# Optimization experiments

Hardware: AMD Instinct MI355X
Metric: run time of the kernel (lower is better)

Reference implementation:

```python
import jax, jax.numpy as jnp
import numpy as np

# Module hyperparameters (init_kwargs)
TOP_K = 0.15          # fraction of pixels kept per row when step_percent=1
IGNORE_INDEX = 255

B, K, N, H, W = 8, 3, 8, 384, 384


def setup_inputs() -> dict:
    key = jax.random.key(0)
    k1, k2 = jax.random.split(key)
    # log-probabilities over K classes (nll_loss expects log-probs)
    logits = jax.random.normal(k1, (B, K, N, H, W), dtype=jnp.float32)
    inp = jax.nn.log_softmax(logits, axis=1)
    target = jax.random.randint(k2, (B, N, H, W), 0, K, dtype=jnp.int32)
    return {"input": inp, "target": target, "step_percent": 1}


def reference(input, target, step_percent):
    b, k, n, h, w = input.shape
    P = h * w
    x = input.reshape(b * n, k, P)           # (BN, K, P)
    t = target.reshape(b * n, P)             # (BN, P)

    # per-pixel NLL with ignore_index (ignored pixels contribute 0)
    mask = t != IGNORE_INDEX
    t_safe = jnp.where(mask, t, 0)
    nll = -jnp.take_along_axis(x, t_safe[:, None, :], axis=1)[:, 0, :]  # (BN, P)
    nll = jnp.where(mask, nll, jnp.zeros((), nll.dtype))

    # static k: step_percent is a Python scalar in the original forward
    sp = min(float(step_percent), 1.0)
    n_top_k = int(sp * TOP_K * P + (1.0 - sp) * P)

    top_k_loss, _ = jax.lax.top_k(nll, n_top_k)  # (BN, n_top_k)
    return jnp.mean(top_k_loss)
```

## Files before the change

### kernel.cpp

```cpp
#include <hip/hip_runtime.h>

#define BN   64
#define KCLS 3
#define PPIX 147456
#define NB1  4096
#define NB3  128
#define BLKS_PER_ROW 36
#define PX_PER_BLK   4096
#define F4_PER_BLK   1024
#define CAP  32768

static const size_t OFF_CAND = 0;
static const size_t OFF_C1   = OFF_CAND + (size_t)BN * CAP * 4;
static const size_t OFF_S1   = OFF_C1 + (size_t)BN * NB1 * 4;
static const size_t OFF_CCNT = OFF_S1 + (size_t)BN * NB1 * 4;
static const size_t OFF_B1   = OFF_CCNT + 256;
static const size_t OFF_R1   = OFF_B1 + 256;
static const size_t OFF_SS   = OFF_R1 + 256;
static const size_t OFF_ACC  = OFF_SS + 512;
static const size_t WS_END   = OFF_ACC + 8;

__device__ __forceinline__ unsigned topk_count(const int* sp_ptr) {
    double sp = (double)sp_ptr[0];
    if (sp > 1.0) sp = 1.0;
    return (unsigned)(sp * 0.15 * (double)PPIX + (1.0 - sp) * (double)PPIX);
}

__device__ __forceinline__ float sel_nll(int t, float a, float b, float c) {
    float lp = (t == 0) ? a : (t == 1) ? b : (t == 2) ? c : 0.0f;
    return fmaxf(-lp, 0.0f);
}

__global__ __launch_bounds__(256) void k_hist1(
    const float* __restrict__ in, const int* __restrict__ tgt,
    unsigned* __restrict__ cnt1, float* __restrict__ sum1)
{
    __shared__ unsigned lc[NB1];
    __shared__ float    ls[NB1];
    const int tid = threadIdx.x;
    for (int i = tid; i < NB1; i += 256) { lc[i] = 0u; ls[i] = 0.0f; }
    __syncthreads();

    const int row   = blockIdx.x / BLKS_PER_ROW;
    const int chunk = blockIdx.x % BLKS_PER_ROW;
    const float4* p0 = (const float4*)(in + (size_t)row * KCLS * PPIX);
    const float4* p1 = p0 + PPIX / 4;
    const float4* p2 = p1 + PPIX / 4;
    const int4*   t4 = (const int4*)(tgt + (size_t)row * PPIX);
    const int base = chunk * (F4_PER_BLK);

    #pragma unroll
    for (int j = 0; j < 4; ++j) {
        const int idx = base + j * 256 + tid;
        const int4   t = t4[idx];
        const float4 a = p0[idx];
        const float4 b = p1[idx];
        const float4 c = p2[idx];
        float v[4];
        v[0] = sel_nll(t.x, a.x, b.x, c.x);
        v[1] = sel_nll(t.y, a.y, b.y, c.y);
        v[2] = sel_nll(t.z, a.z, b.z, c.z);
        v[3] = sel_nll(t.w, a.w, b.w, c.w);
        #pragma unroll
        for (int q = 0; q < 4; ++q) {
            const unsigned key = __float_as_uint(v[q]) >> 19;
            atomicAdd(&lc[key], 1u);
            atomicAdd(&ls[key], v[q]);
        }
    }
    __syncthreads();

    unsigned* gc = cnt1 + (size_t)row * NB1;
    float*    gs = sum1 + (size_t)row * NB1;
    for (int i = tid; i < NB1; i += 256) {
        const unsigned cc = lc[i];
        if (cc) { atomicAdd(&gc[i], cc); atomicAdd(&gs[i], ls[i]); }
    }
}

__global__ __launch_bounds__(256) void k_scan(
    const unsigned* __restrict__ cnt, const float* __restrict__ sum,
    const int* __restrict__ sp_ptr, int* __restrict__ st_b, int* __restrict__ st_r,
    double* __restrict__ st_S)
{
    const int row = blockIdx.x, tid = threadIdx.x;
    __shared__ unsigned csum[256];
    __shared__ double   ssum[256];
    const unsigned* c = cnt + (size_t)row * NB1;
    const float*    s = sum + (size_t)row * NB1;

    unsigned cl[16]; float slv[16];
    unsigned cacc = 0; double sacc = 0.0;
    const int base = tid * 16;
    #pragma unroll
    for (int i = 0; i < 16; ++i) {
        const int bin = NB1 - 1 - (base + i);
        cl[i]  = c[bin];
        slv[i] = s[bin];
        cacc += cl[i];
        sacc += (double)slv[i];
    }
    csum[tid] = cacc; ssum[tid] = sacc;
    __syncthreads();
    for (int off = 1; off < 256; off <<= 1) {
        unsigned cv = 0; double sv = 0.0;
        if (tid >= off) { cv = csum[tid - off]; sv = ssum[tid - off]; }
        __syncthreads();
        csum[tid] += cv; ssum[tid] += sv;
        __syncthreads();
    }

    const unsigned k = topk_count(sp_ptr);
    unsigned cum = tid ? csum[tid - 1] : 0u;
    double   sS  = tid ? ssum[tid - 1] : 0.0;
    #pragma unroll
    for (int i = 0; i < 16; ++i) {
        const unsigned cb = cl[i];
        if (cum < k && cum + cb >= k) {
            st_b[row] = NB1 - 1 - (base + i);
            st_r[row] = (int)(k - cum);
            st_S[row] = sS;
        }
        cum += cb;
        sS  += (double)slv[i];
    }
}

__global__ __launch_bounds__(256) void k_compact(
    const float* __restrict__ in, const int* __restrict__ tgt,
    const int* __restrict__ st_b1, float* __restrict__ cand, int* __restrict__ ccnt)
{
    __shared__ float stage[PX_PER_BLK];
    __shared__ int lcnt, gbase;
    const int tid = threadIdx.x;
    if (tid == 0) lcnt = 0;
    __syncthreads();

    const int row   = blockIdx.x / BLKS_PER_ROW;
    const int chunk = blockIdx.x % BLKS_PER_ROW;
    const unsigned b1 = (unsigned)st_b1[row];
    const float4* p0 = (const float4*)(in + (size_t)row * KCLS * PPIX);
    const float4* p1 = p0 + PPIX / 4;
    const float4* p2 = p1 + PPIX / 4;
    const int4*   t4 = (const int4*)(tgt + (size_t)row * PPIX);
    const int base = chunk * (F4_PER_BLK);

    #pragma unroll
    for (int j = 0; j < 4; ++j) {
        const int idx = base + j * 256 + tid;
        const int4   t = t4[idx];
        const float4 a = p0[idx];
        const float4 b = p1[idx];
        const float4 c = p2[idx];
        float v[4];
        v[0] = sel_nll(t.x, a.x, b.x, c.x);
        v[1] = sel_nll(t.y, a.y, b.y, c.y);
        v[2] = sel_nll(t.z, a.z, b.z, c.z);
        v[3] = sel_nll(t.w, a.w, b.w, c.w);
        #pragma unroll
        for (int q = 0; q < 4; ++q) {
            if ((__float_as_uint(v[q]) >> 19) == b1) {
                const int s = atomicAdd(&lcnt, 1);
                stage[s] = v[q];
            }
        }
    }
    __syncthreads();
    if (tid == 0) gbase = atomicAdd(&ccnt[row], lcnt);
    __syncthreads();
    const int n = lcnt, gb = gbase;
    float* cr = cand + (size_t)row * CAP;
    for (int i = tid; i < n; i += 256) {
        const int pos = gb + i;
        if (pos < CAP) cr[pos] = stage[i];
    }
}

__global__ __launch_bounds__(256) void k_resolve(
    const float* __restrict__ cand, const int* __restrict__ ccnt,
    const int* __restrict__ st_b1, const int* __restrict__ st_r1,
    const double* __restrict__ st_S, double* __restrict__ accum)
{
    __shared__ unsigned lc[NB1];
    __shared__ float    ls[NB1];
    __shared__ unsigned csum[256];
    __shared__ double   ssum[256];
    __shared__ int sb2, sr2;
    __shared__ double sS2;

    const int row = blockIdx.x, tid = threadIdx.x;
    int n = ccnt[row]; if (n > CAP) n = CAP;
    const float* cv = cand + (size_t)row * CAP;

    for (int i = tid; i < NB1; i += 256) { lc[i] = 0u; ls[i] = 0.0f; }
    __syncthreads();
    for (int i = tid; i < n; i += 256) {
        const float v = cv[i];
        const unsigned key = (__float_as_uint(v) >> 7) & 0xFFFu;
        atomicAdd(&lc[key], 1u);
        atomicAdd(&ls[key], v);
    }
    __syncthreads();

    unsigned cl[16]; float slv[16];
    unsigned cacc = 0; double sacc = 0.0;
    const int base = tid * 16;
    #pragma unroll
    for (int i = 0; i < 16; ++i) {
        const int bin = NB1 - 1 - (base + i);
        cl[i]  = lc[bin];
        slv[i] = ls[bin];
        cacc += cl[i];
        sacc += (double)slv[i];
    }
    csum[tid] = cacc; ssum[tid] = sacc;
    __syncthreads();
    for (int off = 1; off < 256; off <<= 1) {
        unsigned cv2 = 0; double sv = 0.0;
        if (tid >= off) { cv2 = csum[tid - off]; sv = ssum[tid - off]; }
        __syncthreads();
        csum[tid] += cv2; ssum[tid] += sv;
        __syncthreads();
    }
    const unsigned k = (unsigned)st_r1[row];
    unsigned cum = tid ? csum[tid - 1] : 0u;
    double   sS  = tid ? ssum[tid - 1] : 0.0;
    #pragma unroll
    for (int i = 0; i < 16; ++i) {
        const unsigned cb = cl[i];
        if (cum < k && cum + cb >= k) {
            sb2 = NB1 - 1 - (base + i);
            sr2 = (int)(k - cum);
            sS2 = sS;
        }
        cum += cb;
        sS  += (double)slv[i];
    }
    __syncthreads();

    const unsigned pref = ((unsigned)st_b1[row] << 12) | (unsigned)sb2;
    if (tid < NB3) { lc[tid] = 0u; ls[tid] = 0.0f; }
    __syncthreads();
    for (int i = tid; i < n; i += 256) {
        const float v = cv[i];
        const unsigned bits = __float_as_uint(v);
        if ((bits >> 7) == pref) {
            atomicAdd(&lc[bits & 0x7Fu], 1u);
            atomicAdd(&ls[bits & 0x7Fu], v);
        }
    }
    __syncthreads();
    if (tid == 0) {
        const unsigned k3 = (unsigned)sr2;
        unsigned cum3 = 0, r3 = 0; int b3 = 0; double S3 = 0.0;
        for (int bin = NB3 - 1; bin >= 0; --bin) {
            const unsigned cb = lc[bin];
            if (cum3 < k3 && cum3 + cb >= k3) { b3 = bin; r3 = k3 - cum3; break; }
            cum3 += cb;
            S3   += (double)ls[bin];
        }
        const float tval = __uint_as_float((pref << 7) | (unsigned)b3);
        const double total = st_S[row] + sS2 + S3 + (double)r3 * (double)tval;
        atomicAdd(accum, total);
    }
}

__global__ void k_out(const double* __restrict__ accum, const int* __restrict__ sp_ptr,
                      float* __restrict__ out)
{
    if (threadIdx.x == 0 && blockIdx.x == 0) {
        const unsigned k = topk_count(sp_ptr);
        out[0] = (float)(accum[0] / ((double)BN * (double)k));
    }
}

extern "C" void kernel_launch(void* const* d_in, const int* in_sizes, int n_in,
                              void* d_out, int out_size, void* d_ws, size_t ws_size,
                              hipStream_t stream)
{
    const float* in  = (const float*)d_in[0];
    const int*   tgt = (const int*)d_in[1];
    const int*   sp  = (const int*)d_in[2];

    char* ws = (char*)d_ws;
    float*    cand  = (float*)(ws + OFF_CAND);
    unsigned* cnt1  = (unsigned*)(ws + OFF_C1);
    float*    sum1  = (float*)(ws + OFF_S1);
    int*      ccnt  = (int*)(ws + OFF_CCNT);
    int*      st_b1 = (int*)(ws + OFF_B1);
    int*      st_r1 = (int*)(ws + OFF_R1);
    double*   st_S  = (double*)(ws + OFF_SS);
    double*   accum = (double*)(ws + OFF_ACC);

    hipMemsetAsync(ws + OFF_C1, 0, WS_END - OFF_C1, stream);

    const int blocks = BN * BLKS_PER_ROW;
    k_hist1  <<<blocks, 256, 0, stream>>>(in, tgt, cnt1, sum1);
    k_scan   <<<BN, 256, 0, stream>>>(cnt1, sum1, sp, st_b1, st_r1, st_S);
    k_compact<<<blocks, 256, 0, stream>>>(in, tgt, st_b1, cand, ccnt);
    k_resolve<<<BN, 256, 0, stream>>>(cand, ccnt, st_b1, st_r1, st_S, accum);
    k_out    <<<1, 64, 0, stream>>>(accum, sp, (float*)d_out);
}
```

Baseline: 279.8 us.

## Materialize per-pixel NLL once and drop float-sum histogram

The histogram pass now writes the computed NLL values to a workspace buffer and counts only bin occupancy, removing the per-bin float atomic sums. The compaction pass reads the 4-byte NLL instead of re-reading the three class planes plus targets, and it accumulates the above-threshold sum in double with a block reduction and one atomic per block. Candidate capacity shrinks to 8192 per row. This trades the extra 37.7 MB write plus read for avoiding a second 16-byte-per-pixel read, and it risks overflowing candidates if a threshold bin holds more than 8192 values.

```diff
diff --git a/kernel.cpp b/kernel.cpp
--- a/kernel.cpp
+++ b/kernel.cpp
@@ -1,24 +1,22 @@
 #include <hip/hip_runtime.h>
 
-#define BN   64
-#define KCLS 3
-#define PPIX 147456
-#define NB1  4096
-#define NB3  128
-#define BLKS_PER_ROW 36
-#define PX_PER_BLK   4096
-#define F4_PER_BLK   1024
-#define CAP  32768
-
-static const size_t OFF_CAND = 0;
+#define BN    64
+#define KCLS  3
+#define PPIX  147456
+#define NB1   4096
+#define NB3   128
+#define BPR   36
+#define PX_BLK 4096
+#define F4_BLK 1024
+#define CAP   8192
+
+static const size_t OFF_NLL  = 0;
+static const size_t OFF_CAND = OFF_NLL + (size_t)BN * PPIX * 4;
 static const size_t OFF_C1   = OFF_CAND + (size_t)BN * CAP * 4;
-static const size_t OFF_S1   = OFF_C1 + (size_t)BN * NB1 * 4;
-static const size_t OFF_CCNT = OFF_S1 + (size_t)BN * NB1 * 4;
-static const size_t OFF_B1   = OFF_CCNT + 256;
-static const size_t OFF_R1   = OFF_B1 + 256;
-static const size_t OFF_SS   = OFF_R1 + 256;
+static const size_t OFF_CCNT = OFF_C1 + (size_t)BN * NB1 * 4;
+static const size_t OFF_SS   = OFF_CCNT + 256;
 static const size_t OFF_ACC  = OFF_SS + 512;
-static const size_t WS_END   = OFF_ACC + 8;
+static const size_t ZERO_END = OFF_ACC + 8;
 
 __device__ __forceinline__ unsigned topk_count(const int* sp_ptr) {
     double sp = (double)sp_ptr[0];
@@ -27,27 +25,27 @@
 }
 
 __device__ __forceinline__ float sel_nll(int t, float a, float b, float c) {
-    float lp = (t == 0) ? a : (t == 1) ? b : (t == 2) ? c : 0.0f;
+    float lp = (t == 0) ? a : ((t == 1) ? b : ((t == 2) ? c : 0.0f));
     return fmaxf(-lp, 0.0f);
 }
 
 __global__ __launch_bounds__(256) void k_hist1(
     const float* __restrict__ in, const int* __restrict__ tgt,
-    unsigned* __restrict__ cnt1, float* __restrict__ sum1)
+    float* __restrict__ nll, unsigned* __restrict__ cnt1)
 {
     __shared__ unsigned lc[NB1];
-    __shared__ float    ls[NB1];
     const int tid = threadIdx.x;
-    for (int i = tid; i < NB1; i += 256) { lc[i] = 0u; ls[i] = 0.0f; }
-    __syncthreads();
-
-    const int row   = blockIdx.x / BLKS_PER_ROW;
-    const int chunk = blockIdx.x % BLKS_PER_ROW;
+    for (int i = tid; i < NB1; i += 256) lc[i] = 0u;
+    __syncthreads();
+
+    const int row   = blockIdx.x / BPR;
+    const int chunk = blockIdx.x % BPR;
     const float4* p0 = (const float4*)(in + (size_t)row * KCLS * PPIX);
     const float4* p1 = p0 + PPIX / 4;
     const float4* p2 = p1 + PPIX / 4;
     const int4*   t4 = (const int4*)(tgt + (size_t)row * PPIX);
-    const int base = chunk * (F4_PER_BLK);
+    float4*       n4 = (float4*)(nll + (size_t)row * PPIX);
+    const int base = chunk * F4_BLK;
 
     #pragma unroll
     for (int j = 0; j < 4; ++j) {
@@ -56,117 +54,107 @@
         const float4 a = p0[idx];
         const float4 b = p1[idx];
         const float4 c = p2[idx];
-        float v[4];
-        v[0] = sel_nll(t.x, a.x, b.x, c.x);
-        v[1] = sel_nll(t.y, a.y, b.y, c.y);
-        v[2] = sel_nll(t.z, a.z, b.z, c.z);
-        v[3] = sel_nll(t.w, a.w, b.w, c.w);
-        #pragma unroll
-        for (int q = 0; q < 4; ++q) {
-            const unsigned key = __float_as_uint(v[q]) >> 19;
-            atomicAdd(&lc[key], 1u);
-            atomicAdd(&ls[key], v[q]);
-        }
+        float4 v;
+        v.x = sel_nll(t.x, a.x, b.x, c.x);
+        v.y = sel_nll(t.y, a.y, b.y, c.y);
+        v.z = sel_nll(t.z, a.z, b.z, c.z);
+        v.w = sel_nll(t.w, a.w, b.w, c.w);
+        n4[idx] = v;
+        atomicAdd(&lc[__float_as_uint(v.x) >> 19], 1u);
+        atomicAdd(&lc[__float_as_uint(v.y) >> 19], 1u);
+        atomicAdd(&lc[__float_as_uint(v.z) >> 19], 1u);
+        atomicAdd(&lc[__float_as_uint(v.w) >> 19], 1u);
     }
     __syncthreads();
 
     unsigned* gc = cnt1 + (size_t)row * NB1;
-    float*    gs = sum1 + (size_t)row * NB1;
     for (int i = tid; i < NB1; i += 256) {
         const unsigned cc = lc[i];
-        if (cc) { atomicAdd(&gc[i], cc); atomicAdd(&gs[i], ls[i]); }
+        if (cc) atomicAdd(&gc[i], cc);
     }
 }
 
 __global__ __launch_bounds__(256) void k_scan(
-    const unsigned* __restrict__ cnt, const float* __restrict__ sum,
-    const int* __restrict__ sp_ptr, int* __restrict__ st_b, int* __restrict__ st_r,
-    double* __restrict__ st_S)
+    const unsigned* __restrict__ cnt, const int* __restrict__ sp_ptr,
+    int* __restrict__ st_b, int* __restrict__ st_r)
 {
     const int row = blockIdx.x, tid = threadIdx.x;
     __shared__ unsigned csum[256];
-    __shared__ double   ssum[256];
     const unsigned* c = cnt + (size_t)row * NB1;
-    const float*    s = sum + (size_t)row * NB1;
-
-    unsigned cl[16]; float slv[16];
-    unsigned cacc = 0; double sacc = 0.0;
+
+    unsigned cl[16]; unsigned cacc = 0;
     const int base = tid * 16;
     #pragma unroll
     for (int i = 0; i < 16; ++i) {
-        const int bin = NB1 - 1 - (base + i);
-        cl[i]  = c[bin];
-        slv[i] = s[bin];
+        cl[i] = c[NB1 - 1 - (base + i)];
         cacc += cl[i];
-        sacc += (double)slv[i];
-    }
-    csum[tid] = cacc; ssum[tid] = sacc;
+    }
+    csum[tid] = cacc;
     __syncthreads();
     for (int off = 1; off < 256; off <<= 1) {
-        unsigned cv = 0; double sv = 0.0;
-        if (tid >= off) { cv = csum[tid - off]; sv = ssum[tid - off]; }
-        __syncthreads();
-        csum[tid] += cv; ssum[tid] += sv;
-        __syncthreads();
-    }
-
+        unsigned t2 = (tid >= off) ? csum[tid - off] : 0u;
+        __syncthreads();
+        csum[tid] += t2;
+        __syncthreads();
+    }
     const unsigned k = topk_count(sp_ptr);
     unsigned cum = tid ? csum[tid - 1] : 0u;
-    double   sS  = tid ? ssum[tid - 1] : 0.0;
     #pragma unroll
     for (int i = 0; i < 16; ++i) {
         const unsigned cb = cl[i];
         if (cum < k && cum + cb >= k) {
             st_b[row] = NB1 - 1 - (base + i);
             st_r[row] = (int)(k - cum);
-            st_S[row] = sS;
         }
         cum += cb;
-        sS  += (double)slv[i];
     }
 }
 
 __global__ __launch_bounds__(256) void k_compact(
-    const float* __restrict__ in, const int* __restrict__ tgt,
-    const int* __restrict__ st_b1, float* __restrict__ cand, int* __restrict__ ccnt)
-{
-    __shared__ float stage[PX_PER_BLK];
+    const float* __restrict__ nll, const int* __restrict__ st_b1,
+    float* __restrict__ cand, int* __restrict__ ccnt, double* __restrict__ st_S)
+{
+    __shared__ float  stage[PX_BLK];
+    __shared__ double dred[256];
     __shared__ int lcnt, gbase;
     const int tid = threadIdx.x;
     if (tid == 0) lcnt = 0;
     __syncthreads();
 
-    const int row   = blockIdx.x / BLKS_PER_ROW;
-    const int chunk = blockIdx.x % BLKS_PER_ROW;
+    const int row   = blockIdx.x / BPR;
+    const int chunk = blockIdx.x % BPR;
     const unsigned b1 = (unsigned)st_b1[row];
-    const float4* p0 = (const float4*)(in + (size_t)row * KCLS * PPIX);
-    const float4* p1 = p0 + PPIX / 4;
-    const float4* p2 = p1 + PPIX / 4;
-    const int4*   t4 = (const int4*)(tgt + (size_t)row * PPIX);
-    const int base = chunk * (F4_PER_BLK);
-
+    const unsigned lo = b1 << 19;
+    const unsigned hi = (b1 + 1u) << 19;
+    const float4* n4 = (const float4*)(nll + (size_t)row * PPIX);
+    const int base = chunk * F4_BLK;
+
+    double acc = 0.0;
     #pragma unroll
     for (int j = 0; j < 4; ++j) {
-        const int idx = base + j * 256 + tid;
-        const int4   t = t4[idx];
-        const float4 a = p0[idx];
-        const float4 b = p1[idx];
-        const float4 c = p2[idx];
-        float v[4];
-        v[0] = sel_nll(t.x, a.x, b.x, c.x);
-        v[1] = sel_nll(t.y, a.y, b.y, c.y);
-        v[2] = sel_nll(t.z, a.z, b.z, c.z);
-        v[3] = sel_nll(t.w, a.w, b.w, c.w);
+        const float4 f = n4[base + j * 256 + tid];
+        const float vv[4] = {f.x, f.y, f.z, f.w};
         #pragma unroll
         for (int q = 0; q < 4; ++q) {
-            if ((__float_as_uint(v[q]) >> 19) == b1) {
+            const unsigned u = __float_as_uint(vv[q]);
+            if (u >= hi) {
+                acc += (double)vv[q];
+            } else if (u >= lo) {
                 const int s = atomicAdd(&lcnt, 1);
-                stage[s] = v[q];
+                stage[s] = vv[q];
             }
         }
     }
-    __syncthreads();
-    if (tid == 0) gbase = atomicAdd(&ccnt[row], lcnt);
+    dred[tid] = acc;
+    __syncthreads();
+    for (int s = 128; s > 0; s >>= 1) {
+        if (tid < s) dred[tid] += dred[tid + s];
+        __syncthreads();
+    }
+    if (tid == 0) {
+        atomicAdd(&st_S[row], dred[0]);
+        gbase = atomicAdd(&ccnt[row], lcnt);
+    }
     __syncthreads();
     const int n = lcnt, gb = gbase;
     float* cr = cand + (size_t)row * CAP;
@@ -283,21 +271,22 @@
     const int*   sp  = (const int*)d_in[2];
 
     char* ws = (char*)d_ws;
+    float*    nll   = (float*)(ws + OFF_NLL);
     float*    cand  = (float*)(ws + OFF_CAND);
     unsigned* cnt1  = (unsigned*)(ws + OFF_C1);
-    float*    sum1  = (float*)(ws + OFF_S1);
     int*      ccnt  = (int*)(ws + OFF_CCNT);
-    int*      st_b1 = (int*)(ws + OFF_B1);
-    int*      st_r1 = (int*)(ws + OFF_R1);
     double*   st_S  = (double*)(ws + OFF_SS);
     double*   accum = (double*)(ws + OFF_ACC);
-
-    hipMemsetAsync(ws + OFF_C1, 0, WS_END - OFF_C1, stream);
-
-    const int blocks = BN * BLKS_PER_ROW;
-    k_hist1  <<<blocks, 256, 0, stream>>>(in, tgt, cnt1, sum1);
-    k_scan   <<<BN, 256, 0, stream>>>(cnt1, sum1, sp, st_b1, st_r1, st_S);
-    k_compact<<<blocks, 256, 0, stream>>>(in, tgt, st_b1, cand, ccnt);
+    int*      st_b1 = (int*)(ws + OFF_CCNT + 64 * 4);
+    st_b1 = (int*)(ws + ZERO_END);
+    int*  st_r1 = (int*)(ws + ZERO_END + 256);
+
+    hipMemsetAsync(ws + OFF_C1, 0, ZERO_END - OFF_C1, stream);
+
+    const int blocks = BN * BPR;
+    k_hist1  <<<blocks, 256, 0, stream>>>(in, tgt, nll, cnt1);
+    k_scan   <<<BN, 256, 0, stream>>>(cnt1, sp, st_b1, st_r1);
+    k_compact<<<blocks, 256, 0, stream>>>(nll, st_b1, cand, ccnt, st_S);
     k_resolve<<<BN, 256, 0, stream>>>(cand, ccnt, st_b1, st_r1, st_S, accum);
     k_out    <<<1, 64, 0, stream>>>(accum, sp, (float*)d_out);
 }
```

After: 254.9 us. 1.1x faster.
